# Optimization experiments

Measured on AMD Instinct MI355X. Metric: run time of the kernel, lower is better.

The kernel has to match this reference:

```python
import jax, jax.numpy as jnp
import numpy as np

B, T, D, H = 8, 512, 1024, 16
DH = D // H  # per-head feature dim (64)


def setup_inputs() -> dict:
    key = jax.random.key(0)
    ks = jax.random.split(key, 10)
    s = 1.0 / np.sqrt(DH)
    inp = {
        "X_data": jax.random.normal(ks[0], (B, T, D), dtype=jnp.float32),
        "mask": jnp.ones((B, T), dtype=jnp.int32),
        # per-head Q/K/V projections (each SelfAttention has its own d_h x d_h weights)
        "Wq": jax.random.normal(ks[1], (H, DH, DH), dtype=jnp.float32) * s,
        "bq": jnp.zeros((H, DH), dtype=jnp.float32),
        "Wk": jax.random.normal(ks[2], (H, DH, DH), dtype=jnp.float32) * s,
        "bk": jnp.zeros((H, DH), dtype=jnp.float32),
        "Wv": jax.random.normal(ks[3], (H, DH, DH), dtype=jnp.float32) * s,
        "bv": jnp.zeros((H, DH), dtype=jnp.float32),
        # AttentionFusion: linear on concatenated head outputs -> len_feature_new
        "Wf": jax.random.normal(ks[4], (D, D), dtype=jnp.float32) * (1.0 / np.sqrt(D)),
        "bf": jnp.zeros((D,), dtype=jnp.float32),
    }
    return inp


def reference(X_data, mask, Wq, bq, Wk, bk, Wv, bv, Wf, bf):
    # Split features into heads: [B, T, H, DH] (equal partitions since D % H == 0)
    Xh = X_data.reshape(B, T, H, DH)
    # Batched per-head projections (replaces the Python loop over heads)
    Q = jnp.einsum("bthd,hde->bhte", Xh, Wq) + bq[None, :, None, :]
    K = jnp.einsum("bthd,hde->bhte", Xh, Wk) + bk[None, :, None, :]
    V = jnp.einsum("bthd,hde->bhte", Xh, Wv) + bv[None, :, None, :]
    scale = 1.0 / jnp.sqrt(jnp.asarray(DH, dtype=Q.dtype))
    scores = jnp.einsum("bhqe,bhke->bhqk", Q, K) * scale  # [B, H, T, T]
    scores = jnp.where(mask[:, None, None, :] > 0, scores, jnp.asarray(-1e9, scores.dtype))
    att = jax.nn.softmax(scores, axis=-1)
    out = jnp.einsum("bhqk,bhke->bhqe", att, V)  # [B, H, T, DH]
    # Concatenate heads (same order as the per-head loop) and fuse
    out = out.transpose(0, 2, 1, 3).reshape(B, T, D)
    fused = out @ Wf + bf  # AttentionFusion linear
    return fused
```

## Files before the change

### kernel.cpp

```cpp
#include <hip/hip_runtime.h>
#include <math.h>

#define B 8
#define T 512
#define D 1024
#define H 16
#define DH 64

typedef __bf16 bf16;
typedef __attribute__((ext_vector_type(8))) __bf16 bf16x8;
typedef __attribute__((ext_vector_type(4))) __bf16 bf16x4;
typedef __attribute__((ext_vector_type(4))) float f32x4;

__device__ __forceinline__ void gld16(const void* g, void* l) {
    __builtin_amdgcn_global_load_lds(
        (const __attribute__((address_space(1))) void*)g,
        (__attribute__((address_space(3))) void*)l, 16, 0, 0);
}


__global__ __launch_bounds__(256) void prep_w(
    const float* __restrict__ Wq, const float* __restrict__ Wk,
    const float* __restrict__ Wv, const float* __restrict__ Wf,
    bf16* __restrict__ WqT, bf16* __restrict__ WkT,
    bf16* __restrict__ WvT, bf16* __restrict__ WfT)
{
    __shared__ bf16 Ts[64 * 72];
    const int blk = blockIdx.x, tid = threadIdx.x;
    if (blk < 48) {
        const int m = blk >> 4, h = blk & 15;
        const float* src = (m == 0 ? Wq : (m == 1 ? Wk : Wv)) + h * 4096;
        bf16* dst = (m == 0 ? WqT : (m == 1 ? WkT : WvT)) + h * 4096;
        for (int i = tid; i < 1024; i += 256) {
            const int d = i >> 4, eq = (i & 15) * 4;
            const float4 w = *(const float4*)(src + d * 64 + eq);
            Ts[(eq + 0) * 72 + d] = (bf16)w.x; Ts[(eq + 1) * 72 + d] = (bf16)w.y;
            Ts[(eq + 2) * 72 + d] = (bf16)w.z; Ts[(eq + 3) * 72 + d] = (bf16)w.w;
        }
        __syncthreads();
        for (int i = tid; i < 512; i += 256) {
            const int e = i >> 3, kc = (i & 7) * 8;
            *(bf16x8*)(dst + e * 64 + kc) = *(const bf16x8*)&Ts[e * 72 + kc];
        }
    } else {
        const int ti = blk - 48, k0 = (ti >> 4) * 64, n0 = (ti & 15) * 64;
        for (int i = tid; i < 1024; i += 256) {
            const int k = i >> 4, nq = (i & 15) * 4;
            const float4 w = *(const float4*)(Wf + (size_t)(k0 + k) * D + n0 + nq);
            Ts[(nq + 0) * 72 + k] = (bf16)w.x; Ts[(nq + 1) * 72 + k] = (bf16)w.y;
            Ts[(nq + 2) * 72 + k] = (bf16)w.z; Ts[(nq + 3) * 72 + k] = (bf16)w.w;
        }
        __syncthreads();
        for (int i = tid; i < 512; i += 256) {
            const int n = i >> 3, kc = (i & 7) * 8;
            *(bf16x8*)(WfT + (size_t)(n0 + n) * D + k0 + kc) = *(const bf16x8*)&Ts[n * 72 + kc];
        }
    }
}

__global__ __launch_bounds__(256) void qkv_mfma(
    const float* __restrict__ X,
    const bf16* __restrict__ WqT, const bf16* __restrict__ WkT,
    const bf16* __restrict__ WvT,
    const float* __restrict__ bq, const float* __restrict__ bk,
    const float* __restrict__ bv,
    bf16* __restrict__ Qb, bf16* __restrict__ Kb, bf16* __restrict__ Vtb)
{
    __shared__ bf16 Xs[128 * 64];
    __shared__ bf16 Wqs[64 * 64], Wks[64 * 64], Wvs[64 * 64];
    __shared__ bf16 Stage[128 * 76];

    const int bh = blockIdx.x & 127, t0 = (blockIdx.x >> 7) * 128;
    const int b = bh >> 4, h = bh & 15;
    const int tid = threadIdx.x, wave = tid >> 6, lane = tid & 63;
    const int quad = lane >> 4, l15 = lane & 15;
    const int lr = lane >> 3, lc = lane & 7;
    const int csw = (lc ^ lr) * 8;

    for (int i = tid; i < 1024; i += 256) {
        const int row = i >> 3, c = i & 7;
        const float* src = X + (size_t)(b * T + t0 + row) * D + h * DH + c * 8;
        const float4 x0 = *(const float4*)src;
        const float4 x1 = *(const float4*)(src + 4);
        bf16x8 t;
        t[0] = (bf16)x0.x; t[1] = (bf16)x0.y; t[2] = (bf16)x0.z; t[3] = (bf16)x0.w;
        t[4] = (bf16)x1.x; t[5] = (bf16)x1.y; t[6] = (bf16)x1.z; t[7] = (bf16)x1.w;
        *(bf16x8*)&Xs[row * 64 + (c ^ (row & 7)) * 8] = t;
    }
    {
        const int r1 = wave * 16;
#pragma unroll
        for (int j = 0; j < 2; ++j) {
            gld16(WqT + (size_t)h * 4096 + (r1 + j * 8 + lr) * 64 + csw, &Wqs[(r1 + j * 8) * 64]);
            gld16(WkT + (size_t)h * 4096 + (r1 + j * 8 + lr) * 64 + csw, &Wks[(r1 + j * 8) * 64]);
            gld16(WvT + (size_t)h * 4096 + (r1 + j * 8 + lr) * 64 + csw, &Wvs[(r1 + j * 8) * 64]);
        }
    }
    __syncthreads();

    bf16x8 af[2][2];
#pragma unroll
    for (int mt = 0; mt < 2; ++mt)
#pragma unroll
        for (int ks = 0; ks < 2; ++ks) {
            const int row = wave * 32 + mt * 16 + l15;
            af[mt][ks] = *(const bf16x8*)&Xs[row * 64 + ((ks * 4 + quad) ^ (l15 & 7)) * 8];
        }

    auto compute = [&](const bf16* Bmat, f32x4 acc[2][4]) {
#pragma unroll
        for (int ks = 0; ks < 2; ++ks) {
            bf16x8 bfr[4];
#pragma unroll
            for (int nt = 0; nt < 4; ++nt)
                bfr[nt] = *(const bf16x8*)&Bmat[(nt * 16 + l15) * 64 + ((ks * 4 + quad) ^ (l15 & 7)) * 8];
#pragma unroll
            for (int mt = 0; mt < 2; ++mt)
#pragma unroll
                for (int nt = 0; nt < 4; ++nt)
                    acc[mt][nt] = __builtin_amdgcn_mfma_f32_16x16x32_bf16(
                        af[mt][ks], bfr[nt], acc[mt][nt], 0, 0, 0);
        }
    };

    const size_t bhTD = (size_t)bh * T * DH;

    {
        f32x4 acc[2][4] = {};
        compute(Wqs, acc);
#pragma unroll
        for (int mt = 0; mt < 2; ++mt)
#pragma unroll
            for (int nt = 0; nt < 4; ++nt) {
                const float bias = bq[h * DH + nt * 16 + l15];
#pragma unroll
                for (int reg = 0; reg < 4; ++reg)
                    Stage[(wave * 32 + mt * 16 + quad * 4 + reg) * 76 + nt * 16 + l15] =
                        (bf16)((acc[mt][nt][reg] + bias) * 0.125f);
            }
        __syncthreads();
        for (int i = tid; i < 1024; i += 256) {
            const int row = i >> 3, c = (i & 7) * 8;
            *(bf16x8*)(Qb + bhTD + (size_t)(t0 + row) * DH + c) = *(const bf16x8*)&Stage[row * 76 + c];
        }
        __syncthreads();
    }
    {
        f32x4 acc[2][4] = {};
        compute(Wks, acc);
#pragma unroll
        for (int mt = 0; mt < 2; ++mt)
#pragma unroll
            for (int nt = 0; nt < 4; ++nt) {
                const float bias = bk[h * DH + nt * 16 + l15];
#pragma unroll
                for (int reg = 0; reg < 4; ++reg)
                    Stage[(wave * 32 + mt * 16 + quad * 4 + reg) * 76 + nt * 16 + l15] =
                        (bf16)(acc[mt][nt][reg] + bias);
            }
        __syncthreads();
        for (int i = tid; i < 1024; i += 256) {
            const int row = i >> 3, c = (i & 7) * 8;
            *(bf16x8*)(Kb + bhTD + (size_t)(t0 + row) * DH + c) = *(const bf16x8*)&Stage[row * 76 + c];
        }
        __syncthreads();
    }
    {
        f32x4 acc[2][4] = {};
        compute(Wvs, acc);
#pragma unroll
        for (int mt = 0; mt < 2; ++mt)
#pragma unroll
            for (int nt = 0; nt < 4; ++nt) {
                const int e = nt * 16 + l15;
                const float bias = bv[h * DH + e];
#pragma unroll
                for (int reg = 0; reg < 4; ++reg) {
                    const int tl = wave * 32 + mt * 16 + quad * 4 + reg;
                    Stage[e * 152 + tl] = (bf16)(acc[mt][nt][reg] + bias);
                }
            }
        __syncthreads();
        for (int i = tid; i < 1024; i += 256) {
            const int e = i >> 4, c = (i & 15) * 8;
            *(bf16x8*)(Vtb + (size_t)bh * DH * T + (size_t)e * T + t0 + c) =
                *(const bf16x8*)&Stage[e * 152 + c];
        }
    }
}

__global__ __launch_bounds__(256) void attn_mfma(
    const bf16* __restrict__ Qb, const bf16* __restrict__ Kb,
    const bf16* __restrict__ Vtb, const int* __restrict__ mask,
    bf16* __restrict__ Ob)
{
    __shared__ bf16 Ks[128 * 64];
    __shared__ bf16 Vts[64 * 128];
    __shared__ bf16 Pl[4][32 * 136];
    __shared__ int msk[128];

    const int bh = blockIdx.x & 127, q0 = (blockIdx.x >> 7) * 128;
    const int b = bh >> 4, h = bh & 15;
    const int tid = threadIdx.x, wave = tid >> 6, lane = tid & 63;
    const int quad = lane >> 4, l15 = lane & 15;
    const int lr = lane >> 3, lc = lane & 7;
    const int csw = (lc ^ lr) * 8;

    const size_t bhTD = (size_t)bh * T * DH;
    const size_t bhDT = (size_t)bh * DH * T;

    bf16x8 qf[2][2];
#pragma unroll
    for (int mt = 0; mt < 2; ++mt)
#pragma unroll
        for (int ks = 0; ks < 2; ++ks)
            qf[mt][ks] = *(const bf16x8*)(Qb + bhTD +
                (size_t)(q0 + wave * 32 + mt * 16 + l15) * DH + ks * 32 + quad * 8);

    f32x4 acc[2][4] = {};
    float lst[2][4] = {};

    for (int kt = 0; kt < 4; ++kt) {
        const int k0 = kt * 128;
        __syncthreads();
        {
            const int r0 = wave * 32;
#pragma unroll
            for (int j = 0; j < 4; ++j)
                gld16(Kb + bhTD + (size_t)(k0 + r0 + j * 8 + lr) * DH + csw,
                      &Ks[(r0 + j * 8) * 64]);
            const int e0 = wave * 16;
#pragma unroll
            for (int j = 0; j < 4; ++j) {
                const int er = j * 4 + (lane >> 4);
                const int csw2 = ((lane & 15) ^ er) * 8;
                gld16(Vtb + bhDT + (size_t)(e0 + er) * T + k0 + csw2,
                      &Vts[(e0 + j * 4) * 128]);
            }
            if (tid < 128) msk[tid] = mask[(size_t)b * T + k0 + tid];
        }
        __syncthreads();

#pragma unroll
        for (int nt = 0; nt < 8; ++nt) {
            const int krow = nt * 16 + l15;
            const bf16x8 kf0 = *(const bf16x8*)&Ks[krow * 64 + ((quad) ^ (l15 & 7)) * 8];
            const bf16x8 kf1 = *(const bf16x8*)&Ks[krow * 64 + ((4 + quad) ^ (l15 & 7)) * 8];
            const int mv = msk[krow];
#pragma unroll
            for (int mt = 0; mt < 2; ++mt) {
                f32x4 s = {};
                s = __builtin_amdgcn_mfma_f32_16x16x32_bf16(qf[mt][0], kf0, s, 0, 0, 0);
                s = __builtin_amdgcn_mfma_f32_16x16x32_bf16(qf[mt][1], kf1, s, 0, 0, 0);
#pragma unroll
                for (int reg = 0; reg < 4; ++reg) {
                    const float p = (mv > 0) ? __expf(s[reg]) : 0.f;
                    lst[mt][reg] += p;
                    Pl[wave][(mt * 16 + quad * 4 + reg) * 136 + nt * 16 + l15] = (bf16)p;
                }
            }
        }
        __builtin_amdgcn_wave_barrier();

#pragma unroll
        for (int kc = 0; kc < 4; ++kc) {
            const bf16x8 pf0 = *(const bf16x8*)&Pl[wave][(l15) * 136 + kc * 32 + quad * 8];
            const bf16x8 pf1 = *(const bf16x8*)&Pl[wave][(16 + l15) * 136 + kc * 32 + quad * 8];
#pragma unroll
            for (int nt = 0; nt < 4; ++nt) {
                const int erow = nt * 16 + l15;
                const bf16x8 vf = *(const bf16x8*)&Vts[erow * 128 + ((kc * 4 + quad) ^ (l15 & 15)) * 8];
                acc[0][nt] = __builtin_amdgcn_mfma_f32_16x16x32_bf16(pf0, vf, acc[0][nt], 0, 0, 0);
                acc[1][nt] = __builtin_amdgcn_mfma_f32_16x16x32_bf16(pf1, vf, acc[1][nt], 0, 0, 0);
            }
        }
    }

    __syncthreads();
    bf16* Ostage = &Pl[0][0];
#pragma unroll
    for (int mt = 0; mt < 2; ++mt)
#pragma unroll
        for (int reg = 0; reg < 4; ++reg) {
            float l = lst[mt][reg];
            l += __shfl_xor(l, 1);
            l += __shfl_xor(l, 2);
            l += __shfl_xor(l, 4);
            l += __shfl_xor(l, 8);
            const float inv = 1.f / l;
            const int row = wave * 32 + mt * 16 + quad * 4 + reg;
#pragma unroll
            for (int nt = 0; nt < 4; ++nt)
                Ostage[row * 76 + nt * 16 + l15] = (bf16)(acc[mt][nt][reg] * inv);
        }
    __syncthreads();
    for (int i = tid; i < 1024; i += 256) {
        const int row = i >> 3, c = (i & 7) * 8;
        *(bf16x8*)(Ob + ((size_t)b * T + q0 + row) * D + h * DH + c) =
            *(const bf16x8*)&Ostage[row * 76 + c];
    }
}

__global__ __launch_bounds__(256) void fuse_mfma(
    const bf16* __restrict__ Ob, const bf16* __restrict__ WfT,
    const float* __restrict__ bfv, float* __restrict__ out)
{
    __shared__ bf16 smem[128 * 128 + 64 * 128];
    bf16* As = smem;
    bf16* Bs = smem + 128 * 128;

    const int col0 = blockIdx.x * 64;
    const int row0 = blockIdx.y * 128;
    const int tid = threadIdx.x, wave = tid >> 6, lane = tid & 63;
    const int quad = lane >> 4, l15 = lane & 15;
    const int lr4 = lane >> 4, lc16 = lane & 15;
    const int wm = wave * 32;

    f32x4 acc[2][4] = {};

    for (int k0 = 0; k0 < D; k0 += 128) {
        __syncthreads();
#pragma unroll
        for (int j = 0; j < 8; ++j) {
            const int row = wm + j * 4 + lr4;
            gld16(Ob + (size_t)(row0 + row) * D + k0 + ((lc16 ^ (row & 15)) * 8),
                  &As[(wm + j * 4) * 128]);
        }
#pragma unroll
        for (int j = 0; j < 4; ++j) {
            const int row = wave * 16 + j * 4 + lr4;
            gld16(WfT + (size_t)(col0 + row) * D + k0 + ((lc16 ^ (row & 15)) * 8),
                  &Bs[(wave * 16 + j * 4) * 128]);
        }
        __syncthreads();
#pragma unroll
        for (int ks = 0; ks < 4; ++ks) {
            bf16x8 af[2], bfr[4];
#pragma unroll
            for (int mt = 0; mt < 2; ++mt) {
                const int row = wm + mt * 16 + l15;
                af[mt] = *(const bf16x8*)&As[row * 128 + ((ks * 4 + quad) ^ l15) * 8];
            }
#pragma unroll
            for (int nt = 0; nt < 4; ++nt)
                bfr[nt] = *(const bf16x8*)&Bs[(nt * 16 + l15) * 128 + ((ks * 4 + quad) ^ l15) * 8];
#pragma unroll
            for (int mt = 0; mt < 2; ++mt)
#pragma unroll
                for (int nt = 0; nt < 4; ++nt)
                    acc[mt][nt] = __builtin_amdgcn_mfma_f32_16x16x32_bf16(af[mt], bfr[nt], acc[mt][nt], 0, 0, 0);
        }
    }

    __syncthreads();
    float* Ofs = (float*)smem;
    float bias[4];
#pragma unroll
    for (int nt = 0; nt < 4; ++nt) bias[nt] = bfv[col0 + nt * 16 + l15];
#pragma unroll
    for (int mt = 0; mt < 2; ++mt)
#pragma unroll
        for (int reg = 0; reg < 4; ++reg) {
            const int row = wm + mt * 16 + quad * 4 + reg;
#pragma unroll
            for (int nt = 0; nt < 4; ++nt)
                Ofs[row * 68 + nt * 16 + l15] = acc[mt][nt][reg] + bias[nt];
        }
    __syncthreads();
    for (int i = tid; i < 2048; i += 256) {
        const int row = i >> 4, c = (i & 15) * 4;
        *(float4*)(out + (size_t)(row0 + row) * D + col0 + c) = *(const float4*)&Ofs[row * 68 + c];
    }
}

extern "C" void kernel_launch(void* const* d_in, const int* in_sizes, int n_in,
                              void* d_out, int out_size, void* d_ws, size_t ws_size,
                              hipStream_t stream) {
    const float* X   = (const float*)d_in[0];
    const int* mask  = (const int*)d_in[1];
    const float* Wq  = (const float*)d_in[2];
    const float* bq  = (const float*)d_in[3];
    const float* Wk  = (const float*)d_in[4];
    const float* bk  = (const float*)d_in[5];
    const float* Wv  = (const float*)d_in[6];
    const float* bv  = (const float*)d_in[7];
    const float* Wf  = (const float*)d_in[8];
    const float* bfv = (const float*)d_in[9];
    float* out = (float*)d_out;

    bf16* wsb = (bf16*)d_ws;
    const size_t QN = (size_t)B * H * T * DH;
    bf16* Qb  = wsb;
    bf16* Kb  = wsb + QN;
    bf16* Vtb = wsb + 2 * QN;
    bf16* Ob  = wsb + 3 * QN;
    bf16* WfT = wsb + 4 * QN;
    bf16* WqT = WfT + (size_t)D * D;
    bf16* WkT = WqT + H * DH * DH;
    bf16* WvT = WkT + H * DH * DH;

    prep_w<<<dim3(304), 256, 0, stream>>>(Wq, Wk, Wv, Wf, WqT, WkT, WvT, WfT);
    qkv_mfma<<<dim3(B * H * 4), 256, 0, stream>>>(X, WqT, WkT, WvT, bq, bk, bv, Qb, Kb, Vtb);
    attn_mfma<<<dim3(B * H * 4), 256, 0, stream>>>(Qb, Kb, Vtb, mask, Ob);
    fuse_mfma<<<dim3(D / 64, (B * T) / 128), 256, 0, stream>>>(Ob, WfT, bfv, out);
}
```

Measured before the change: 129.3 us.

## Fuse QKV projection into attention kernel, recomputing K/V per query block

Merges the separate QKV projection and attention kernels into one. Each block projects its own Q tile and recomputes K and V for every 64-key tile directly from X, so intermediates never touch global memory. This removes the Q/K/Vt workspace writes and reads and one kernel launch. In exchange, K/V projection is repeated once per query block, X is re-read redundantly, and extra barriers are added inside the key loop.

```diff
diff --git a/kernel.cpp b/kernel.cpp
--- a/kernel.cpp
+++ b/kernel.cpp
@@ -9,7 +9,6 @@
 
 typedef __bf16 bf16;
 typedef __attribute__((ext_vector_type(8))) __bf16 bf16x8;
-typedef __attribute__((ext_vector_type(4))) __bf16 bf16x4;
 typedef __attribute__((ext_vector_type(4))) float f32x4;
 
 __device__ __forceinline__ void gld16(const void* g, void* l) {
@@ -58,146 +57,26 @@
     }
 }
 
-__global__ __launch_bounds__(256) void qkv_mfma(
-    const float* __restrict__ X,
+__global__ __launch_bounds__(256, 3) void qkv_attn(
+    const float* __restrict__ X, const int* __restrict__ mask,
     const bf16* __restrict__ WqT, const bf16* __restrict__ WkT,
     const bf16* __restrict__ WvT,
     const float* __restrict__ bq, const float* __restrict__ bk,
     const float* __restrict__ bv,
-    bf16* __restrict__ Qb, bf16* __restrict__ Kb, bf16* __restrict__ Vtb)
-{
-    __shared__ bf16 Xs[128 * 64];
-    __shared__ bf16 Wqs[64 * 64], Wks[64 * 64], Wvs[64 * 64];
-    __shared__ bf16 Stage[128 * 76];
-
-    const int bh = blockIdx.x & 127, t0 = (blockIdx.x >> 7) * 128;
-    const int b = bh >> 4, h = bh & 15;
-    const int tid = threadIdx.x, wave = tid >> 6, lane = tid & 63;
-    const int quad = lane >> 4, l15 = lane & 15;
-    const int lr = lane >> 3, lc = lane & 7;
-    const int csw = (lc ^ lr) * 8;
-
-    for (int i = tid; i < 1024; i += 256) {
-        const int row = i >> 3, c = i & 7;
-        const float* src = X + (size_t)(b * T + t0 + row) * D + h * DH + c * 8;
-        const float4 x0 = *(const float4*)src;
-        const float4 x1 = *(const float4*)(src + 4);
-        bf16x8 t;
-        t[0] = (bf16)x0.x; t[1] = (bf16)x0.y; t[2] = (bf16)x0.z; t[3] = (bf16)x0.w;
-        t[4] = (bf16)x1.x; t[5] = (bf16)x1.y; t[6] = (bf16)x1.z; t[7] = (bf16)x1.w;
-        *(bf16x8*)&Xs[row * 64 + (c ^ (row & 7)) * 8] = t;
-    }
-    {
-        const int r1 = wave * 16;
-#pragma unroll
-        for (int j = 0; j < 2; ++j) {
-            gld16(WqT + (size_t)h * 4096 + (r1 + j * 8 + lr) * 64 + csw, &Wqs[(r1 + j * 8) * 64]);
-            gld16(WkT + (size_t)h * 4096 + (r1 + j * 8 + lr) * 64 + csw, &Wks[(r1 + j * 8) * 64]);
-            gld16(WvT + (size_t)h * 4096 + (r1 + j * 8 + lr) * 64 + csw, &Wvs[(r1 + j * 8) * 64]);
-        }
-    }
-    __syncthreads();
-
-    bf16x8 af[2][2];
-#pragma unroll
-    for (int mt = 0; mt < 2; ++mt)
-#pragma unroll
-        for (int ks = 0; ks < 2; ++ks) {
-            const int row = wave * 32 + mt * 16 + l15;
-            af[mt][ks] = *(const bf16x8*)&Xs[row * 64 + ((ks * 4 + quad) ^ (l15 & 7)) * 8];
-        }
-
-    auto compute = [&](const bf16* Bmat, f32x4 acc[2][4]) {
-#pragma unroll
-        for (int ks = 0; ks < 2; ++ks) {
-            bf16x8 bfr[4];
-#pragma unroll
-            for (int nt = 0; nt < 4; ++nt)
-                bfr[nt] = *(const bf16x8*)&Bmat[(nt * 16 + l15) * 64 + ((ks * 4 + quad) ^ (l15 & 7)) * 8];
-#pragma unroll
-            for (int mt = 0; mt < 2; ++mt)
-#pragma unroll
-                for (int nt = 0; nt < 4; ++nt)
-                    acc[mt][nt] = __builtin_amdgcn_mfma_f32_16x16x32_bf16(
-                        af[mt][ks], bfr[nt], acc[mt][nt], 0, 0, 0);
-        }
-    };
-
-    const size_t bhTD = (size_t)bh * T * DH;
-
-    {
-        f32x4 acc[2][4] = {};
-        compute(Wqs, acc);
-#pragma unroll
-        for (int mt = 0; mt < 2; ++mt)
-#pragma unroll
-            for (int nt = 0; nt < 4; ++nt) {
-                const float bias = bq[h * DH + nt * 16 + l15];
-#pragma unroll
-                for (int reg = 0; reg < 4; ++reg)
-                    Stage[(wave * 32 + mt * 16 + quad * 4 + reg) * 76 + nt * 16 + l15] =
-                        (bf16)((acc[mt][nt][reg] + bias) * 0.125f);
-            }
-        __syncthreads();
-        for (int i = tid; i < 1024; i += 256) {
-            const int row = i >> 3, c = (i & 7) * 8;
-            *(bf16x8*)(Qb + bhTD + (size_t)(t0 + row) * DH + c) = *(const bf16x8*)&Stage[row * 76 + c];
-        }
-        __syncthreads();
-    }
-    {
-        f32x4 acc[2][4] = {};
-        compute(Wks, acc);
-#pragma unroll
-        for (int mt = 0; mt < 2; ++mt)
-#pragma unroll
-            for (int nt = 0; nt < 4; ++nt) {
-                const float bias = bk[h * DH + nt * 16 + l15];
-#pragma unroll
-                for (int reg = 0; reg < 4; ++reg)
-                    Stage[(wave * 32 + mt * 16 + quad * 4 + reg) * 76 + nt * 16 + l15] =
-                        (bf16)(acc[mt][nt][reg] + bias);
-            }
-        __syncthreads();
-        for (int i = tid; i < 1024; i += 256) {
-            const int row = i >> 3, c = (i & 7) * 8;
-            *(bf16x8*)(Kb + bhTD + (size_t)(t0 + row) * DH + c) = *(const bf16x8*)&Stage[row * 76 + c];
-        }
-        __syncthreads();
-    }
-    {
-        f32x4 acc[2][4] = {};
-        compute(Wvs, acc);
-#pragma unroll
-        for (int mt = 0; mt < 2; ++mt)
-#pragma unroll
-            for (int nt = 0; nt < 4; ++nt) {
-                const int e = nt * 16 + l15;
-                const float bias = bv[h * DH + e];
-#pragma unroll
-                for (int reg = 0; reg < 4; ++reg) {
-                    const int tl = wave * 32 + mt * 16 + quad * 4 + reg;
-                    Stage[e * 152 + tl] = (bf16)(acc[mt][nt][reg] + bias);
-                }
-            }
-        __syncthreads();
-        for (int i = tid; i < 1024; i += 256) {
-            const int e = i >> 4, c = (i & 15) * 8;
-            *(bf16x8*)(Vtb + (size_t)bh * DH * T + (size_t)e * T + t0 + c) =
-                *(const bf16x8*)&Stage[e * 152 + c];
-        }
-    }
-}
-
-__global__ __launch_bounds__(256) void attn_mfma(
-    const bf16* __restrict__ Qb, const bf16* __restrict__ Kb,
-    const bf16* __restrict__ Vtb, const int* __restrict__ mask,
     bf16* __restrict__ Ob)
 {
-    __shared__ bf16 Ks[128 * 64];
-    __shared__ bf16 Vts[64 * 128];
-    __shared__ bf16 Pl[4][32 * 136];
-    __shared__ int msk[128];
+    __shared__ __align__(16) char smem[53504];
+    bf16* Wks = (bf16*)(smem);
+    bf16* Wvs = (bf16*)(smem + 8192);
+    bf16* Ks  = (bf16*)(smem + 16384);
+    bf16* Vts = (bf16*)(smem + 25600);
+    bf16* Pl  = (bf16*)(smem + 34816);
+    int*  msk = (int*)(smem + 53248);
+    bf16* Wqs   = Ks;
+    bf16* Xq    = Vts;
+    bf16* Stage = Pl;
+    bf16* Xkt   = Pl;
+    bf16* Ostage = Pl;
 
     const int bh = blockIdx.x & 127, q0 = (blockIdx.x >> 7) * 128;
     const int b = bh >> 4, h = bh & 15;
@@ -206,78 +85,169 @@
     const int lr = lane >> 3, lc = lane & 7;
     const int csw = (lc ^ lr) * 8;
 
-    const size_t bhTD = (size_t)bh * T * DH;
-    const size_t bhDT = (size_t)bh * DH * T;
-
+    float bqr[4], bkr[4], bvr[4];
+#pragma unroll
+    for (int nt = 0; nt < 4; ++nt) {
+        bqr[nt] = bq[h * DH + nt * 16 + l15];
+        bkr[nt] = bk[h * DH + nt * 16 + l15];
+        bvr[nt] = bv[h * DH + nt * 16 + l15];
+    }
+
+    {
+        const int r1 = wave * 16;
+#pragma unroll
+        for (int j = 0; j < 2; ++j) {
+            gld16(WqT + (size_t)h * 4096 + (r1 + j * 8 + lr) * 64 + csw, &Wqs[(r1 + j * 8) * 64]);
+            gld16(WkT + (size_t)h * 4096 + (r1 + j * 8 + lr) * 64 + csw, &Wks[(r1 + j * 8) * 64]);
+            gld16(WvT + (size_t)h * 4096 + (r1 + j * 8 + lr) * 64 + csw, &Wvs[(r1 + j * 8) * 64]);
+        }
+    }
+    for (int i = tid; i < 1024; i += 256) {
+        const int row = i >> 3, c = i & 7;
+        const float* src = X + (size_t)(b * T + q0 + row) * D + h * DH + c * 8;
+        const float4 x0 = *(const float4*)src;
+        const float4 x1 = *(const float4*)(src + 4);
+        bf16x8 t;
+        t[0] = (bf16)x0.x; t[1] = (bf16)x0.y; t[2] = (bf16)x0.z; t[3] = (bf16)x0.w;
+        t[4] = (bf16)x1.x; t[5] = (bf16)x1.y; t[6] = (bf16)x1.z; t[7] = (bf16)x1.w;
+        *(bf16x8*)&Xq[row * 64 + ((c ^ (row & 7)) * 8)] = t;
+    }
+    __syncthreads();
+
+    {
+        f32x4 accQ[2][4] = {};
+#pragma unroll
+        for (int ks = 0; ks < 2; ++ks) {
+            bf16x8 af[2], bfr[4];
+#pragma unroll
+            for (int mt = 0; mt < 2; ++mt) {
+                const int row = wave * 32 + mt * 16 + l15;
+                af[mt] = *(const bf16x8*)&Xq[row * 64 + (((ks * 4 + quad) ^ (l15 & 7)) * 8)];
+            }
+#pragma unroll
+            for (int nt = 0; nt < 4; ++nt)
+                bfr[nt] = *(const bf16x8*)&Wqs[(nt * 16 + l15) * 64 + (((ks * 4 + quad) ^ (l15 & 7)) * 8)];
+#pragma unroll
+            for (int mt = 0; mt < 2; ++mt)
+#pragma unroll
+                for (int nt = 0; nt < 4; ++nt)
+                    accQ[mt][nt] = __builtin_amdgcn_mfma_f32_16x16x32_bf16(af[mt], bfr[nt], accQ[mt][nt], 0, 0, 0);
+        }
+        __syncthreads();
+#pragma unroll
+        for (int mt = 0; mt < 2; ++mt)
+#pragma unroll
+            for (int nt = 0; nt < 4; ++nt)
+#pragma unroll
+                for (int reg = 0; reg < 4; ++reg)
+                    Stage[(wave * 32 + mt * 16 + quad * 4 + reg) * 72 + nt * 16 + l15] =
+                        (bf16)((accQ[mt][nt][reg] + bqr[nt]) * 0.125f);
+        __builtin_amdgcn_wave_barrier();
+    }
     bf16x8 qf[2][2];
 #pragma unroll
     for (int mt = 0; mt < 2; ++mt)
 #pragma unroll
         for (int ks = 0; ks < 2; ++ks)
-            qf[mt][ks] = *(const bf16x8*)(Qb + bhTD +
-                (size_t)(q0 + wave * 32 + mt * 16 + l15) * DH + ks * 32 + quad * 8);
+            qf[mt][ks] = *(const bf16x8*)&Stage[(wave * 32 + mt * 16 + l15) * 72 + ks * 32 + quad * 8];
 
     f32x4 acc[2][4] = {};
     float lst[2][4] = {};
 
-    for (int kt = 0; kt < 4; ++kt) {
-        const int k0 = kt * 128;
-        __syncthreads();
+    for (int kt = 0; kt < 8; ++kt) {
+        const int k0 = kt * 64;
+        __syncthreads();
+        if (tid < 64) msk[tid] = mask[(size_t)b * T + k0 + tid];
         {
-            const int r0 = wave * 32;
-#pragma unroll
-            for (int j = 0; j < 4; ++j)
-                gld16(Kb + bhTD + (size_t)(k0 + r0 + j * 8 + lr) * DH + csw,
-                      &Ks[(r0 + j * 8) * 64]);
-            const int e0 = wave * 16;
-#pragma unroll
-            for (int j = 0; j < 4; ++j) {
-                const int er = j * 4 + (lane >> 4);
-                const int csw2 = ((lane & 15) ^ er) * 8;
-                gld16(Vtb + bhDT + (size_t)(e0 + er) * T + k0 + csw2,
-                      &Vts[(e0 + j * 4) * 128]);
+            const int krow = wave * 16 + (lane >> 2);
+            const int c0 = (lane & 3) * 2;
+            const float* src = X + (size_t)(b * T + k0 + krow) * D + h * DH + c0 * 8;
+            const float4 x0 = *(const float4*)src;
+            const float4 x1 = *(const float4*)(src + 4);
+            const float4 x2 = *(const float4*)(src + 8);
+            const float4 x3 = *(const float4*)(src + 12);
+            bf16x8 t0, t1;
+            t0[0] = (bf16)x0.x; t0[1] = (bf16)x0.y; t0[2] = (bf16)x0.z; t0[3] = (bf16)x0.w;
+            t0[4] = (bf16)x1.x; t0[5] = (bf16)x1.y; t0[6] = (bf16)x1.z; t0[7] = (bf16)x1.w;
+            t1[0] = (bf16)x2.x; t1[1] = (bf16)x2.y; t1[2] = (bf16)x2.z; t1[3] = (bf16)x2.w;
+            t1[4] = (bf16)x3.x; t1[5] = (bf16)x3.y; t1[6] = (bf16)x3.z; t1[7] = (bf16)x3.w;
+            *(bf16x8*)&Xkt[krow * 64 + ((c0 ^ (krow & 7)) * 8)] = t0;
+            *(bf16x8*)&Xkt[krow * 64 + (((c0 + 1) ^ (krow & 7)) * 8)] = t1;
+        }
+        __builtin_amdgcn_wave_barrier();
+
+        {
+            bf16x8 afkv[2];
+#pragma unroll
+            for (int ks = 0; ks < 2; ++ks)
+                afkv[ks] = *(const bf16x8*)&Xkt[(wave * 16 + l15) * 64 + (((ks * 4 + quad) ^ (l15 & 7)) * 8)];
+            f32x4 accK[4] = {}, accV[4] = {};
+#pragma unroll
+            for (int ks = 0; ks < 2; ++ks)
+#pragma unroll
+                for (int nt = 0; nt < 4; ++nt) {
+                    const bf16x8 bk8 = *(const bf16x8*)&Wks[(nt * 16 + l15) * 64 + (((ks * 4 + quad) ^ (l15 & 7)) * 8)];
+                    accK[nt] = __builtin_amdgcn_mfma_f32_16x16x32_bf16(afkv[ks], bk8, accK[nt], 0, 0, 0);
+                    const bf16x8 bv8 = *(const bf16x8*)&Wvs[(nt * 16 + l15) * 64 + (((ks * 4 + quad) ^ (l15 & 7)) * 8)];
+                    accV[nt] = __builtin_amdgcn_mfma_f32_16x16x32_bf16(afkv[ks], bv8, accV[nt], 0, 0, 0);
+                }
+#pragma unroll
+            for (int nt = 0; nt < 4; ++nt)
+#pragma unroll
+                for (int reg = 0; reg < 4; ++reg) {
+                    const int key = wave * 16 + quad * 4 + reg;
+                    const int e = nt * 16 + l15;
+                    Ks[key * 72 + e] = (bf16)(accK[nt][reg] + bkr[nt]);
+                    Vts[e * 72 + key] = (bf16)(accV[nt][reg] + bvr[nt]);
+                }
+        }
+        __syncthreads();
+
+        bf16* Plw = Pl + wave * (32 * 72);
+        {
+            bf16x8 kf[4][2];
+#pragma unroll
+            for (int nt = 0; nt < 4; ++nt)
+#pragma unroll
+                for (int ks = 0; ks < 2; ++ks)
+                    kf[nt][ks] = *(const bf16x8*)&Ks[(nt * 16 + l15) * 72 + ks * 32 + quad * 8];
+            int mv[4];
+#pragma unroll
+            for (int nt = 0; nt < 4; ++nt) mv[nt] = msk[nt * 16 + l15];
+#pragma unroll
+            for (int mt = 0; mt < 2; ++mt) {
+                f32x4 s[4] = {};
+#pragma unroll
+                for (int ks = 0; ks < 2; ++ks)
+#pragma unroll
+                    for (int nt = 0; nt < 4; ++nt)
+                        s[nt] = __builtin_amdgcn_mfma_f32_16x16x32_bf16(qf[mt][ks], kf[nt][ks], s[nt], 0, 0, 0);
+#pragma unroll
+                for (int nt = 0; nt < 4; ++nt)
+#pragma unroll
+                    for (int reg = 0; reg < 4; ++reg) {
+                        const float p = (mv[nt] > 0) ? __expf(s[nt][reg]) : 0.f;
+                        lst[mt][reg] += p;
+                        Plw[(mt * 16 + quad * 4 + reg) * 72 + nt * 16 + l15] = (bf16)p;
+                    }
             }
-            if (tid < 128) msk[tid] = mask[(size_t)b * T + k0 + tid];
-        }
-        __syncthreads();
-
-#pragma unroll
-        for (int nt = 0; nt < 8; ++nt) {
-            const int krow = nt * 16 + l15;
-            const bf16x8 kf0 = *(const bf16x8*)&Ks[krow * 64 + ((quad) ^ (l15 & 7)) * 8];
-            const bf16x8 kf1 = *(const bf16x8*)&Ks[krow * 64 + ((4 + quad) ^ (l15 & 7)) * 8];
-            const int mv = msk[krow];
-#pragma unroll
-            for (int mt = 0; mt < 2; ++mt) {
-                f32x4 s = {};
-                s = __builtin_amdgcn_mfma_f32_16x16x32_bf16(qf[mt][0], kf0, s, 0, 0, 0);
-                s = __builtin_amdgcn_mfma_f32_16x16x32_bf16(qf[mt][1], kf1, s, 0, 0, 0);
-#pragma unroll
-                for (int reg = 0; reg < 4; ++reg) {
-                    const float p = (mv > 0) ? __expf(s[reg]) : 0.f;
-                    lst[mt][reg] += p;
-                    Pl[wave][(mt * 16 + quad * 4 + reg) * 136 + nt * 16 + l15] = (bf16)p;
-                }
-            }
         }
         __builtin_amdgcn_wave_barrier();
 
 #pragma unroll
-        for (int kc = 0; kc < 4; ++kc) {
-            const bf16x8 pf0 = *(const bf16x8*)&Pl[wave][(l15) * 136 + kc * 32 + quad * 8];
-            const bf16x8 pf1 = *(const bf16x8*)&Pl[wave][(16 + l15) * 136 + kc * 32 + quad * 8];
+        for (int kc = 0; kc < 2; ++kc) {
+            const bf16x8 pf0 = *(const bf16x8*)&Plw[(l15) * 72 + kc * 32 + quad * 8];
+            const bf16x8 pf1 = *(const bf16x8*)&Plw[(16 + l15) * 72 + kc * 32 + quad * 8];
 #pragma unroll
             for (int nt = 0; nt < 4; ++nt) {
-                const int erow = nt * 16 + l15;
-                const bf16x8 vf = *(const bf16x8*)&Vts[erow * 128 + ((kc * 4 + quad) ^ (l15 & 15)) * 8];
+                const bf16x8 vf = *(const bf16x8*)&Vts[(nt * 16 + l15) * 72 + kc * 32 + quad * 8];
                 acc[0][nt] = __builtin_amdgcn_mfma_f32_16x16x32_bf16(pf0, vf, acc[0][nt], 0, 0, 0);
                 acc[1][nt] = __builtin_amdgcn_mfma_f32_16x16x32_bf16(pf1, vf, acc[1][nt], 0, 0, 0);
             }
         }
     }
 
-    __syncthreads();
-    bf16* Ostage = &Pl[0][0];
+    __builtin_amdgcn_wave_barrier();
 #pragma unroll
     for (int mt = 0; mt < 2; ++mt)
 #pragma unroll
@@ -291,13 +261,13 @@
             const int row = wave * 32 + mt * 16 + quad * 4 + reg;
 #pragma unroll
             for (int nt = 0; nt < 4; ++nt)
-                Ostage[row * 76 + nt * 16 + l15] = (bf16)(acc[mt][nt][reg] * inv);
+                Ostage[row * 72 + nt * 16 + l15] = (bf16)(acc[mt][nt][reg] * inv);
         }
     __syncthreads();
     for (int i = tid; i < 1024; i += 256) {
         const int row = i >> 3, c = (i & 7) * 8;
         *(bf16x8*)(Ob + ((size_t)b * T + q0 + row) * D + h * DH + c) =
-            *(const bf16x8*)&Ostage[row * 76 + c];
+            *(const bf16x8*)&Ostage[row * 72 + c];
     }
 }
 
@@ -390,17 +360,13 @@
 
     bf16* wsb = (bf16*)d_ws;
     const size_t QN = (size_t)B * H * T * DH;
-    bf16* Qb  = wsb;
-    bf16* Kb  = wsb + QN;
-    bf16* Vtb = wsb + 2 * QN;
-    bf16* Ob  = wsb + 3 * QN;
-    bf16* WfT = wsb + 4 * QN;
+    bf16* Ob  = wsb;
+    bf16* WfT = wsb + QN;
     bf16* WqT = WfT + (size_t)D * D;
     bf16* WkT = WqT + H * DH * DH;
     bf16* WvT = WkT + H * DH * DH;
 
     prep_w<<<dim3(304), 256, 0, stream>>>(Wq, Wk, Wv, Wf, WqT, WkT, WvT, WfT);
-    qkv_mfma<<<dim3(B * H * 4), 256, 0, stream>>>(X, WqT, WkT, WvT, bq, bk, bv, Qb, Kb, Vtb);
-    attn_mfma<<<dim3(B * H * 4), 256, 0, stream>>>(Qb, Kb, Vtb, mask, Ob);
+    qkv_attn<<<dim3(512), 256, 0, stream>>>(X, mask, WqT, WkT, WvT, bq, bk, bv, Ob);
     fuse_mfma<<<dim3(D / 64, (B * T) / 128), 256, 0, stream>>>(Ob, WfT, bfv, out);
 }
```

After: 130.6 us. About the same (+1.0%).
